# Kernel tuning notes

Measured on AMD Instinct MI355X. Metric: run time of the kernel, lower is better.

Reference implementation:

```python
import jax, jax.numpy as jnp
import numpy as np

N_HEAD = 16


def setup_inputs() -> dict:
    key = jax.random.key(0)
    ks = jax.random.split(key, 8)
    B, T, S, C = 8, 1024, 1024, 1024
    s = 0.02
    return {
        "x": jax.random.normal(ks[0], (B, T, C), jnp.float32),
        "feature": jax.random.normal(ks[1], (B, S, C), jnp.float32),
        "Wc": jax.random.normal(ks[2], (C, C), jnp.float32) * s,
        "bc": jax.random.normal(ks[3], (C,), jnp.float32) * s,
        "Wf": jax.random.normal(ks[4], (2 * C, C), jnp.float32) * s,
        "bf": jax.random.normal(ks[5], (2 * C,), jnp.float32) * s,
        "Wp": jax.random.normal(ks[6], (C, C), jnp.float32) * s,
        "bp": jax.random.normal(ks[7], (C,), jnp.float32) * s,
    }


def reference(x, feature, Wc, bc, Wf, bf, Wp, bp):
    B, T, C = x.shape
    S = feature.shape[1]
    H = N_HEAD
    d = C // H
    # q projection: [B,T,C] -> [B,H,T,d]
    q = (x @ Wc.T + bc).reshape(B, T, H, d).transpose(0, 2, 1, 3)
    # k,v from feature: [B,S,2C] split
    kv = feature @ Wf.T + bf
    k, v = kv[..., :C], kv[..., C:]
    k = k.reshape(B, S, H, d).transpose(0, 2, 1, 3)
    v = v.reshape(B, S, H, d).transpose(0, 2, 1, 3)
    scale = 1.0 / jnp.sqrt(jnp.asarray(d, x.dtype))
    att = jnp.einsum("bhtd,bhsd->bhts", q, k) * scale
    # asymmetric tril mask: allow column s <= row t
    mask = jnp.arange(T)[:, None] >= jnp.arange(S)[None, :]  # [T,S]
    att = jnp.where(mask[None, None], att, -jnp.inf)
    att = jax.nn.softmax(att, axis=-1)
    out = jnp.einsum("bhts,bhsd->bhtd", att, v)
    out = out.transpose(0, 2, 1, 3).reshape(B, T, C)
    return out @ Wp.T + bp
```

## Files before the change

kernel.cpp:

```cpp
#include <hip/hip_runtime.h>

typedef __attribute__((ext_vector_type(4))) float  f32x4;
typedef __attribute__((ext_vector_type(8))) short  bf8;
typedef __attribute__((ext_vector_type(4))) unsigned short us4;

#define AS1 __attribute__((address_space(1)))
#define AS3 __attribute__((address_space(3)))

static __device__ __forceinline__ unsigned short f2b(float f) {
  unsigned u = __builtin_bit_cast(unsigned, f);
  u += 0x7FFFu + ((u >> 16) & 1u);
  return (unsigned short)(u >> 16);
}

__global__ __launch_bounds__(256) void cvt_kernel(const float* __restrict__ in,
                                                  unsigned short* __restrict__ out,
                                                  int n) {
  int i = blockIdx.x * 256 + threadIdx.x;
  int idx = i << 2;
  if (idx >= n) return;
  f32x4 v = *(const f32x4*)(in + idx);
  us4 o;
  o[0] = f2b(v[0]); o[1] = f2b(v[1]); o[2] = f2b(v[2]); o[3] = f2b(v[3]);
  *(us4*)(out + idx) = o;
}

template<int EPI>
__global__ __launch_bounds__(256) void gemm_bt(const unsigned short* __restrict__ A,
                                               const unsigned short* __restrict__ Bt,
                                               const float* __restrict__ bias,
                                               unsigned short* __restrict__ out0,
                                               unsigned short* __restrict__ out1,
                                               float* __restrict__ outf,
                                               int M, int N, int K) {
  __shared__ unsigned short As[128 * 32];
  __shared__ unsigned short Bs[128 * 32];
  const int tid = threadIdx.x;
  const int lane = tid & 63, wid = tid >> 6;
  const int l15 = lane & 15, lg = lane >> 4;
  const int bm = blockIdx.y, bn = blockIdx.x;
  const int wr = wid >> 1, wc = wid & 1;
  f32x4 acc[4][4] = {};

  const unsigned short* Ab = A  + (size_t)bm * 128 * K;
  const unsigned short* Bb = Bt + (size_t)bn * 128 * K;

  for (int k0 = 0; k0 < K; k0 += 32) {
    __syncthreads();
#pragma unroll
    for (int r = 0; r < 2; ++r) {
      int c = r * 256 + tid;
      int row = c >> 2, c8 = c & 3;
      const unsigned short* ga = Ab + (size_t)row * K + k0 + c8 * 8;
      const unsigned short* gb = Bb + (size_t)row * K + k0 + c8 * 8;
      AS3 unsigned short* la = (AS3 unsigned short*)As + (r * 256 + wid * 64) * 8;
      AS3 unsigned short* lb = (AS3 unsigned short*)Bs + (r * 256 + wid * 64) * 8;
      __builtin_amdgcn_global_load_lds((const AS1 void*)ga, (AS3 void*)la, 16, 0, 0);
      __builtin_amdgcn_global_load_lds((const AS1 void*)gb, (AS3 void*)lb, 16, 0, 0);
    }
    __syncthreads();
    bf8 af[4], bv[4];
#pragma unroll
    for (int m = 0; m < 4; ++m)
      af[m] = *(const bf8*)&As[(wr * 64 + m * 16 + l15) * 32 + lg * 8];
#pragma unroll
    for (int n = 0; n < 4; ++n)
      bv[n] = *(const bf8*)&Bs[(wc * 64 + n * 16 + l15) * 32 + lg * 8];
#pragma unroll
    for (int m = 0; m < 4; ++m)
#pragma unroll
      for (int n = 0; n < 4; ++n)
        acc[m][n] = __builtin_amdgcn_mfma_f32_16x16x32_bf16(af[m], bv[n], acc[m][n], 0, 0, 0);
  }

  float bvs[4];
#pragma unroll
  for (int n = 0; n < 4; ++n) bvs[n] = bias[bn * 128 + wc * 64 + n * 16 + l15];

#pragma unroll
  for (int m = 0; m < 4; ++m) {
    int gm0 = bm * 128 + wr * 64 + m * 16 + lg * 4;
#pragma unroll
    for (int n = 0; n < 4; ++n) {
      int gn = bn * 128 + wc * 64 + n * 16 + l15;
#pragma unroll
      for (int j = 0; j < 4; ++j) {
        float val = acc[m][n][j] + bvs[n];
        int gm = gm0 + j;
        if (EPI == 0) {
          int b = gm >> 10, t = gm & 1023, h = gn >> 6, dd = gn & 63;
          out0[((((size_t)b * 16 + h) << 10) + t) * 64 + dd] = f2b(val);
        } else if (EPI == 1) {
          int b = gm >> 10, s = gm & 1023;
          if (gn < 1024) {
            int h = gn >> 6, dd = gn & 63;
            out0[((((size_t)b * 16 + h) << 10) + s) * 64 + dd] = f2b(val);
          } else {
            int g2 = gn - 1024, h = g2 >> 6, dd = g2 & 63;
            out1[((((size_t)b * 16 + h) << 10) + s) * 64 + dd] = f2b(val);
          }
        } else {
          outf[(size_t)gm * N + gn] = val;
        }
      }
    }
  }
}

__global__ __launch_bounds__(256) void attn_kernel(const unsigned short* __restrict__ q,
                                                   const unsigned short* __restrict__ k,
                                                   const unsigned short* __restrict__ v,
                                                   unsigned short* __restrict__ out) {
  const int qt = blockIdx.x;
  const int bh = blockIdx.y;
  const int tid = threadIdx.x, lane = tid & 63, wid = tid >> 6;
  const int l15 = lane & 15, lg = lane >> 4;
  __shared__ unsigned short Pl[4][16 * 64];
  __shared__ unsigned short Vt[64 * 72];

  const size_t kvbase = (size_t)bh * 1024 * 64;
  const int q0 = qt * 64;

  bf8 qf[2];
  {
    const unsigned short* qp = q + kvbase + (size_t)(q0 + wid * 16 + l15) * 64;
    qf[0] = *(const bf8*)(qp + lg * 8);
    qf[1] = *(const bf8*)(qp + 32 + lg * 8);
  }
  f32x4 o[4] = {};
  float mrow[4] = {-1e30f, -1e30f, -1e30f, -1e30f};
  float lrow[4] = {0.f, 0.f, 0.f, 0.f};

  for (int st = 0; st <= qt; ++st) {
    const int s0 = st * 64;
    __syncthreads();
#pragma unroll
    for (int r = 0; r < 2; ++r) {
      int c = r * 256 + tid;
      int s = c >> 3, d8 = c & 7;
      bf8 vv = *(const bf8*)(v + kvbase + (size_t)(s0 + s) * 64 + d8 * 8);
#pragma unroll
      for (int i = 0; i < 8; ++i)
        Vt[(d8 * 8 + i) * 72 + s] = (unsigned short)vv[i];
    }
    float att[4][4];
#pragma unroll
    for (int n = 0; n < 4; ++n) {
      f32x4 a = {0.f, 0.f, 0.f, 0.f};
      const unsigned short* kp = k + kvbase + (size_t)(s0 + n * 16 + l15) * 64;
      a = __builtin_amdgcn_mfma_f32_16x16x32_bf16(qf[0], *(const bf8*)(kp + lg * 8), a, 0, 0, 0);
      a = __builtin_amdgcn_mfma_f32_16x16x32_bf16(qf[1], *(const bf8*)(kp + 32 + lg * 8), a, 0, 0, 0);
#pragma unroll
      for (int j = 0; j < 4; ++j) att[n][j] = a[j] * 0.125f;
    }
    if (st == qt) {
#pragma unroll
      for (int n = 0; n < 4; ++n)
#pragma unroll
        for (int j = 0; j < 4; ++j)
          if (n * 16 + l15 > wid * 16 + lg * 4 + j) att[n][j] = -1e30f;
    }
    float pm[4], mnew[4], al[4], ps[4];
#pragma unroll
    for (int j = 0; j < 4; ++j)
      pm[j] = fmaxf(fmaxf(att[0][j], att[1][j]), fmaxf(att[2][j], att[3][j]));
#pragma unroll
    for (int sh = 1; sh < 16; sh <<= 1)
#pragma unroll
      for (int j = 0; j < 4; ++j) pm[j] = fmaxf(pm[j], __shfl_xor(pm[j], sh));
#pragma unroll
    for (int j = 0; j < 4; ++j) {
      mnew[j] = fmaxf(mrow[j], pm[j]);
      al[j] = __expf(mrow[j] - mnew[j]);
      ps[j] = 0.f;
    }
#pragma unroll
    for (int n = 0; n < 4; ++n)
#pragma unroll
      for (int j = 0; j < 4; ++j) {
        float p = __expf(att[n][j] - mnew[j]);
        ps[j] += p;
        Pl[wid][(lg * 4 + j) * 64 + n * 16 + l15] = f2b(p);
      }
#pragma unroll
    for (int sh = 1; sh < 16; sh <<= 1)
#pragma unroll
      for (int j = 0; j < 4; ++j) ps[j] += __shfl_xor(ps[j], sh);
#pragma unroll
    for (int j = 0; j < 4; ++j) {
      lrow[j] = lrow[j] * al[j] + ps[j];
      mrow[j] = mnew[j];
    }
#pragma unroll
    for (int n = 0; n < 4; ++n) {
      f32x4 t = o[n];
#pragma unroll
      for (int j = 0; j < 4; ++j) t[j] *= al[j];
      o[n] = t;
    }
    __syncthreads();
#pragma unroll
    for (int n = 0; n < 4; ++n) {
#pragma unroll
      for (int kk = 0; kk < 2; ++kk) {
        bf8 pa = *(const bf8*)&Pl[wid][l15 * 64 + kk * 32 + lg * 8];
        bf8 vb = *(const bf8*)&Vt[(n * 16 + l15) * 72 + kk * 32 + lg * 8];
        o[n] = __builtin_amdgcn_mfma_f32_16x16x32_bf16(pa, vb, o[n], 0, 0, 0);
      }
    }
  }
  const int b = bh >> 4, h = bh & 15;
#pragma unroll
  for (int n = 0; n < 4; ++n)
#pragma unroll
    for (int j = 0; j < 4; ++j) {
      float val = o[n][j] / lrow[j];
      int t = q0 + wid * 16 + lg * 4 + j;
      out[((size_t)b * 1024 + t) * 1024 + h * 64 + n * 16 + l15] = f2b(val);
    }
}

extern "C" void kernel_launch(void* const* d_in, const int* in_sizes, int n_in,
                              void* d_out, int out_size, void* d_ws, size_t ws_size,
                              hipStream_t stream) {
  const float* x   = (const float*)d_in[0];
  const float* ft  = (const float*)d_in[1];
  const float* Wc  = (const float*)d_in[2];
  const float* bc  = (const float*)d_in[3];
  const float* Wf  = (const float*)d_in[4];
  const float* bff = (const float*)d_in[5];
  const float* Wp  = (const float*)d_in[6];
  const float* bp  = (const float*)d_in[7];
  float* out = (float*)d_out;

  const size_t MEG = 1024 * 1024;
  unsigned short* xb  = (unsigned short*)d_ws;
  unsigned short* fb  = xb  + 8 * MEG;
  unsigned short* Wcb = fb  + 8 * MEG;
  unsigned short* Wfb = Wcb + 1 * MEG;
  unsigned short* Wpb = Wfb + 2 * MEG;
  unsigned short* qb  = Wpb + 1 * MEG;
  unsigned short* kb  = qb  + 8 * MEG;
  unsigned short* vb  = kb  + 8 * MEG;
  unsigned short* ab  = vb  + 8 * MEG;

  cvt_kernel<<<8192, 256, 0, stream>>>(x,  xb,  8 * MEG);
  cvt_kernel<<<8192, 256, 0, stream>>>(ft, fb,  8 * MEG);
  cvt_kernel<<<1024, 256, 0, stream>>>(Wc, Wcb, 1 * MEG);
  cvt_kernel<<<2048, 256, 0, stream>>>(Wf, Wfb, 2 * MEG);
  cvt_kernel<<<1024, 256, 0, stream>>>(Wp, Wpb, 1 * MEG);

  gemm_bt<0><<<dim3(8, 64), 256, 0, stream>>>(xb, Wcb, bc, qb, nullptr, nullptr, 8192, 1024, 1024);
  gemm_bt<1><<<dim3(16, 64), 256, 0, stream>>>(fb, Wfb, bff, kb, vb, nullptr, 8192, 2048, 1024);
  attn_kernel<<<dim3(16, 128), 256, 0, stream>>>(qb, kb, vb, ab);
  gemm_bt<2><<<dim3(8, 64), 256, 0, stream>>>(ab, Wpb, bp, nullptr, nullptr, out, 8192, 1024, 1024);
}
```

Before: 424.8 us.

## Pre-transpose V and load K/V fragments directly into registers in attention

```diff
diff --git a/kernel.cpp b/kernel.cpp
--- a/kernel.cpp
+++ b/kernel.cpp
@@ -3,6 +3,7 @@
 typedef __attribute__((ext_vector_type(4))) float  f32x4;
 typedef __attribute__((ext_vector_type(8))) short  bf8;
 typedef __attribute__((ext_vector_type(4))) unsigned short us4;
+typedef __attribute__((ext_vector_type(8))) unsigned short us8;
 
 #define AS1 __attribute__((address_space(1)))
 #define AS3 __attribute__((address_space(3)))
@@ -107,18 +108,43 @@
   }
 }
 
+__global__ __launch_bounds__(256) void vtrans_kernel(const unsigned short* __restrict__ v,
+                                                     unsigned short* __restrict__ vt) {
+  __shared__ unsigned short T[64][72];
+  const int bh = blockIdx.y;
+  const int s0 = blockIdx.x * 64;
+  const int tid = threadIdx.x;
+  const size_t base = (size_t)bh * 65536;
+#pragma unroll
+  for (int r = 0; r < 2; ++r) {
+    int c = r * 256 + tid;
+    int s = c >> 3, d8 = c & 7;
+    bf8 x = *(const bf8*)(v + base + (size_t)(s0 + s) * 64 + d8 * 8);
+    *(bf8*)&T[s][d8 * 8] = x;
+  }
+  __syncthreads();
+#pragma unroll
+  for (int r = 0; r < 2; ++r) {
+    int c = r * 256 + tid;
+    int dd = c & 63, sc = (c >> 6);
+    us8 y;
+#pragma unroll
+    for (int i = 0; i < 8; ++i) y[i] = T[sc * 8 + i][dd];
+    *(us8*)(vt + base + (size_t)dd * 1024 + s0 + sc * 8) = y;
+  }
+}
+
 __global__ __launch_bounds__(256) void attn_kernel(const unsigned short* __restrict__ q,
                                                    const unsigned short* __restrict__ k,
-                                                   const unsigned short* __restrict__ v,
+                                                   const unsigned short* __restrict__ vt,
                                                    unsigned short* __restrict__ out) {
-  const int qt = blockIdx.x;
+  const int qt = 15 - blockIdx.x;
   const int bh = blockIdx.y;
   const int tid = threadIdx.x, lane = tid & 63, wid = tid >> 6;
   const int l15 = lane & 15, lg = lane >> 4;
-  __shared__ unsigned short Pl[4][16 * 64];
-  __shared__ unsigned short Vt[64 * 72];
-
-  const size_t kvbase = (size_t)bh * 1024 * 64;
+  __shared__ unsigned short Pl[4][16 * 72];
+
+  const size_t kvbase = (size_t)bh * 65536;
   const int q0 = qt * 64;
 
   bf8 qf[2];
@@ -133,34 +159,46 @@
 
   for (int st = 0; st <= qt; ++st) {
     const int s0 = st * 64;
-    __syncthreads();
-#pragma unroll
-    for (int r = 0; r < 2; ++r) {
-      int c = r * 256 + tid;
-      int s = c >> 3, d8 = c & 7;
-      bf8 vv = *(const bf8*)(v + kvbase + (size_t)(s0 + s) * 64 + d8 * 8);
-#pragma unroll
-      for (int i = 0; i < 8; ++i)
-        Vt[(d8 * 8 + i) * 72 + s] = (unsigned short)vv[i];
-    }
+    const int nmax = (st == qt) ? (wid + 1) : 4;
+    const unsigned short* kp0 = k + kvbase + (size_t)s0 * 64;
+    const unsigned short* vp0 = vt + kvbase + s0;
+
+    bf8 kf[4][2], vf[4][2];
+#pragma unroll
+    for (int n = 0; n < 4; ++n)
+      if (n < nmax) {
+        const unsigned short* kp = kp0 + (n * 16 + l15) * 64 + lg * 8;
+        kf[n][0] = *(const bf8*)kp;
+        kf[n][1] = *(const bf8*)(kp + 32);
+      }
+#pragma unroll
+    for (int kk = 0; kk < 2; ++kk)
+      if (kk * 2 < nmax)
+#pragma unroll
+        for (int n = 0; n < 4; ++n)
+          vf[n][kk] = *(const bf8*)(vp0 + (size_t)(n * 16 + l15) * 1024 + kk * 32 + lg * 8);
+
     float att[4][4];
 #pragma unroll
     for (int n = 0; n < 4; ++n) {
-      f32x4 a = {0.f, 0.f, 0.f, 0.f};
-      const unsigned short* kp = k + kvbase + (size_t)(s0 + n * 16 + l15) * 64;
-      a = __builtin_amdgcn_mfma_f32_16x16x32_bf16(qf[0], *(const bf8*)(kp + lg * 8), a, 0, 0, 0);
-      a = __builtin_amdgcn_mfma_f32_16x16x32_bf16(qf[1], *(const bf8*)(kp + 32 + lg * 8), a, 0, 0, 0);
-#pragma unroll
-      for (int j = 0; j < 4; ++j) att[n][j] = a[j] * 0.125f;
-    }
-    if (st == qt) {
-#pragma unroll
-      for (int n = 0; n < 4; ++n)
-#pragma unroll
-        for (int j = 0; j < 4; ++j)
-          if (n * 16 + l15 > wid * 16 + lg * 4 + j) att[n][j] = -1e30f;
-    }
-    float pm[4], mnew[4], al[4], ps[4];
+      if (n < nmax) {
+        f32x4 a = {0.f, 0.f, 0.f, 0.f};
+        a = __builtin_amdgcn_mfma_f32_16x16x32_bf16(qf[0], kf[n][0], a, 0, 0, 0);
+        a = __builtin_amdgcn_mfma_f32_16x16x32_bf16(qf[1], kf[n][1], a, 0, 0, 0);
+#pragma unroll
+        for (int j = 0; j < 4; ++j) att[n][j] = a[j] * 0.125f;
+        if (st == qt) {
+#pragma unroll
+          for (int j = 0; j < 4; ++j)
+            if (n * 16 + l15 > wid * 16 + lg * 4 + j) att[n][j] = -1e30f;
+        }
+      } else {
+#pragma unroll
+        for (int j = 0; j < 4; ++j) att[n][j] = -1e30f;
+      }
+    }
+
+    float pm[4];
 #pragma unroll
     for (int j = 0; j < 4; ++j)
       pm[j] = fmaxf(fmaxf(att[0][j], att[1][j]), fmaxf(att[2][j], att[3][j]));
@@ -168,47 +206,45 @@
     for (int sh = 1; sh < 16; sh <<= 1)
 #pragma unroll
       for (int j = 0; j < 4; ++j) pm[j] = fmaxf(pm[j], __shfl_xor(pm[j], sh));
+    float al[4], ps[4];
 #pragma unroll
     for (int j = 0; j < 4; ++j) {
-      mnew[j] = fmaxf(mrow[j], pm[j]);
-      al[j] = __expf(mrow[j] - mnew[j]);
+      float mnew = fmaxf(mrow[j], pm[j]);
+      al[j] = __expf(mrow[j] - mnew);
+      mrow[j] = mnew;
       ps[j] = 0.f;
     }
 #pragma unroll
     for (int n = 0; n < 4; ++n)
 #pragma unroll
       for (int j = 0; j < 4; ++j) {
-        float p = __expf(att[n][j] - mnew[j]);
-        ps[j] += p;
-        Pl[wid][(lg * 4 + j) * 64 + n * 16 + l15] = f2b(p);
+        float e = __expf(att[n][j] - mrow[j]);
+        ps[j] += e;
+        Pl[wid][(lg * 4 + j) * 72 + n * 16 + l15] = f2b(e);
       }
 #pragma unroll
     for (int sh = 1; sh < 16; sh <<= 1)
 #pragma unroll
       for (int j = 0; j < 4; ++j) ps[j] += __shfl_xor(ps[j], sh);
 #pragma unroll
-    for (int j = 0; j < 4; ++j) {
-      lrow[j] = lrow[j] * al[j] + ps[j];
-      mrow[j] = mnew[j];
-    }
+    for (int j = 0; j < 4; ++j) lrow[j] = lrow[j] * al[j] + ps[j];
 #pragma unroll
     for (int n = 0; n < 4; ++n) {
       f32x4 t = o[n];
-#pragma unroll
-      for (int j = 0; j < 4; ++j) t[j] *= al[j];
+      t[0] *= al[0]; t[1] *= al[1]; t[2] *= al[2]; t[3] *= al[3];
       o[n] = t;
     }
-    __syncthreads();
-#pragma unroll
-    for (int n = 0; n < 4; ++n) {
-#pragma unroll
-      for (int kk = 0; kk < 2; ++kk) {
-        bf8 pa = *(const bf8*)&Pl[wid][l15 * 64 + kk * 32 + lg * 8];
-        bf8 vb = *(const bf8*)&Vt[(n * 16 + l15) * 72 + kk * 32 + lg * 8];
-        o[n] = __builtin_amdgcn_mfma_f32_16x16x32_bf16(pa, vb, o[n], 0, 0, 0);
-      }
-    }
-  }
+
+#pragma unroll
+    for (int kk = 0; kk < 2; ++kk)
+      if (kk * 2 < nmax) {
+        bf8 pa = *(const bf8*)&Pl[wid][l15 * 72 + kk * 32 + lg * 8];
+#pragma unroll
+        for (int n = 0; n < 4; ++n)
+          o[n] = __builtin_amdgcn_mfma_f32_16x16x32_bf16(pa, vf[n][kk], o[n], 0, 0, 0);
+      }
+  }
+
   const int b = bh >> 4, h = bh & 15;
 #pragma unroll
   for (int n = 0; n < 4; ++n)
@@ -252,6 +288,7 @@
 
   gemm_bt<0><<<dim3(8, 64), 256, 0, stream>>>(xb, Wcb, bc, qb, nullptr, nullptr, 8192, 1024, 1024);
   gemm_bt<1><<<dim3(16, 64), 256, 0, stream>>>(fb, Wfb, bff, kb, vb, nullptr, 8192, 2048, 1024);
-  attn_kernel<<<dim3(16, 128), 256, 0, stream>>>(qb, kb, vb, ab);
+  vtrans_kernel<<<dim3(16, 128), 256, 0, stream>>>(vb, xb);
+  attn_kernel<<<dim3(16, 128), 256, 0, stream>>>(qb, kb, xb, ab);
   gemm_bt<2><<<dim3(8, 64), 256, 0, stream>>>(ab, Wpb, bp, nullptr, nullptr, out, 8192, 1024, 1024);
 }
```

Measured after the change: 491.1 us. 1.16x slower.
